# Performance work log

Hardware: AMD Instinct MI355X
Metric: run time of the kernel (lower is better)

## Reference

```python
import jax, jax.numpy as jnp
import numpy as np

T = 2048          # tokens (single causal prefill sequence)
H = 4096          # hidden_size
NH = 32           # num query heads
NKV = 8           # num kv heads (GQA)
HD = H // NH      # head_dim = 128
ROPE_THETA = 500000.0
Q_SIZE = NH * HD
KV_SIZE = NKV * HD


def setup_inputs() -> dict:
    key = jax.random.key(0)
    k1, k2, k3 = jax.random.split(key, 3)
    return {
        "positions": jnp.arange(T, dtype=jnp.int32),
        "hidden_states": jax.random.normal(k1, (T, H), dtype=jnp.float32) * 0.02,
        "w_qkv": jax.random.normal(k2, (H, Q_SIZE + 2 * KV_SIZE), dtype=jnp.float32) * (1.0 / np.sqrt(H)),
        "w_o": jax.random.normal(k3, (Q_SIZE, H), dtype=jnp.float32) * (1.0 / np.sqrt(Q_SIZE)),
    }


def _apply_rope(x, positions):
    # x: [T, heads, HD]; neox-style (non-interleaved) RoPE as in get_rope
    half = HD // 2
    inv_freq = 1.0 / (ROPE_THETA ** (jnp.arange(0, half, dtype=jnp.float32) / half * 1.0))
    # note: standard llama uses arange(0, HD, 2)/HD == arange(half)/half
    freqs = positions.astype(jnp.float32)[:, None] * inv_freq[None, :]   # [T, half]
    cos = jnp.cos(freqs)[:, None, :]  # [T, 1, half]
    sin = jnp.sin(freqs)[:, None, :]
    x1, x2 = x[..., :half], x[..., half:]
    return jnp.concatenate([x1 * cos - x2 * sin, x2 * cos + x1 * sin], axis=-1).astype(x.dtype)


def reference(positions, hidden_states, w_qkv, w_o):
    # qkv_proj (no bias)
    qkv = hidden_states @ w_qkv                               # [T, 6144]
    q, k, v = jnp.split(qkv, [Q_SIZE, Q_SIZE + KV_SIZE], axis=-1)
    q = q.reshape(T, NH, HD)
    k = k.reshape(T, NKV, HD)
    v = v.reshape(T, NKV, HD)

    # fused RoPE on q and k (k would be written rotated into the KV cache)
    q = _apply_rope(q, positions)
    k = _apply_rope(k, positions)

    # GQA: expand kv heads to query heads
    group = NH // NKV
    k_rep = jnp.repeat(k, group, axis=1)                      # [T, NH, HD]
    v_rep = jnp.repeat(v, group, axis=1)

    scale = HD ** -0.5
    scores = jnp.einsum('qhd,shd->hqs', q, k_rep) * scale     # [NH, T, T]
    causal = jnp.tril(jnp.ones((T, T), dtype=bool))
    scores = jnp.where(causal[None], scores, jnp.finfo(scores.dtype).min)
    probs = jax.nn.softmax(scores, axis=-1)
    attn = jnp.einsum('hqs,shd->qhd', probs, v_rep)           # [T, NH, HD]

    out = attn.reshape(T, Q_SIZE) @ w_o                       # o_proj
    return out
```

## Files before the change

kernel.cpp:

```cpp
#include <hip/hip_runtime.h>
#include <cstdint>
#include <cstddef>

#define T_SEQ 2048
#define H_DIM 4096
#define NH 32
#define NKV 8
#define HD 128
#define QKV_N 6144
#define Q_SIZE 4096
#define KV_SIZE 1024

typedef __attribute__((ext_vector_type(8))) short bf16x8;
typedef __attribute__((ext_vector_type(4))) short short4v;
typedef __attribute__((ext_vector_type(4))) float f32x4;

__device__ __forceinline__ short f2bf(float f) {
  union { float f; uint32_t u; } v; v.f = f;
  uint32_t r = v.u + 0x7fffu + ((v.u >> 16) & 1u);
  return (short)(r >> 16);
}

__device__ __forceinline__ void gload_lds16(const void* g, void* l) {
  __builtin_amdgcn_global_load_lds((const __attribute__((address_space(1))) void*)g,
                                   (__attribute__((address_space(3))) void*)l,
                                   16, 0, 0);
}

__global__ __launch_bounds__(256) void cvt_bf16_kernel(const float* __restrict__ in,
                                                       short* __restrict__ out, int n4) {
  int i = blockIdx.x * 256 + threadIdx.x;
  if (i < n4) {
    float4 v = ((const float4*)in)[i];
    short4v s;
    s.x = f2bf(v.x); s.y = f2bf(v.y); s.z = f2bf(v.z); s.w = f2bf(v.w);
    ((short4v*)out)[i] = s;
  }
}

__global__ __launch_bounds__(256) void transpose_cvt_kernel(const float* __restrict__ in,
                                                            short* __restrict__ out,
                                                            int rows, int cols) {
  __shared__ float tile[32][33];
  int bx = blockIdx.x * 32;
  int by = blockIdx.y * 32;
  int x = threadIdx.x, y = threadIdx.y;
#pragma unroll
  for (int i = 0; i < 32; i += 8)
    tile[y + i][x] = in[(size_t)(by + y + i) * cols + bx + x];
  __syncthreads();
#pragma unroll
  for (int i = 0; i < 32; i += 8)
    out[(size_t)(bx + y + i) * rows + by + x] = f2bf(tile[x][y + i]);
}

__global__ __launch_bounds__(256) void gemm_bt_kernel(const short* __restrict__ A,
                                                      const short* __restrict__ Bt,
                                                      float* __restrict__ C,
                                                      int M, int N, int K) {
  __shared__ short As[128 * 32];
  __shared__ short Bs[128 * 32];
  int tid = threadIdx.x;
  int w = tid >> 6, lane = tid & 63;
  int quad = lane >> 4, l16 = lane & 15;
  int wm = (w >> 1) * 64, wn = (w & 1) * 64;
  int bm = blockIdx.y * 128, bn = blockIdx.x * 128;
  f32x4 acc[4][4] = {};
  for (int kk = 0; kk < K; kk += 32) {
    __syncthreads();
#pragma unroll
    for (int p = 0; p < 2; ++p) {
      int e = (p * 256 + tid) * 8;
      int row = e >> 5, kc = e & 31;
      gload_lds16(A + (size_t)(bm + row) * K + kk + kc, As + e);
      gload_lds16(Bt + (size_t)(bn + row) * K + kk + kc, Bs + e);
    }
    __syncthreads();
    bf16x8 af[4], bfr[4];
#pragma unroll
    for (int mi = 0; mi < 4; ++mi)
      af[mi] = *(const bf16x8*)(As + (wm + mi * 16 + l16) * 32 + quad * 8);
#pragma unroll
    for (int ni = 0; ni < 4; ++ni)
      bfr[ni] = *(const bf16x8*)(Bs + (wn + ni * 16 + l16) * 32 + quad * 8);
#pragma unroll
    for (int mi = 0; mi < 4; ++mi)
#pragma unroll
      for (int ni = 0; ni < 4; ++ni)
        acc[mi][ni] = __builtin_amdgcn_mfma_f32_16x16x32_bf16(af[mi], bfr[ni], acc[mi][ni], 0, 0, 0);
  }
#pragma unroll
  for (int mi = 0; mi < 4; ++mi)
#pragma unroll
    for (int ni = 0; ni < 4; ++ni) {
      int r0 = bm + wm + mi * 16 + quad * 4;
      int c0 = bn + wn + ni * 16 + l16;
#pragma unroll
      for (int r = 0; r < 4; ++r)
        C[(size_t)(r0 + r) * N + c0] = acc[mi][ni][r];
    }
}

__global__ __launch_bounds__(256) void qkv_gemm_kernel(const short* __restrict__ A,
                                                       const short* __restrict__ Bt,
                                                       const int* __restrict__ positions,
                                                       short* __restrict__ qb,
                                                       short* __restrict__ kb,
                                                       short* __restrict__ vt) {
  __shared__ short As[128 * 32];
  __shared__ short Bs[128 * 32];
  const int K = H_DIM;
  int tid = threadIdx.x;
  int w = tid >> 6, lane = tid & 63;
  int quad = lane >> 4, l16 = lane & 15;
  int wm = (w >> 1) * 64;
  int cgb = (w & 1) * 32;
  int cb = blockIdx.x;
  int bm = blockIdx.y * 128, bn = cb * 128;
  f32x4 acc[4][4] = {};
  for (int kk = 0; kk < K; kk += 32) {
    __syncthreads();
#pragma unroll
    for (int p = 0; p < 2; ++p) {
      int e = (p * 256 + tid) * 8;
      int row = e >> 5, kc = e & 31;
      gload_lds16(A + (size_t)(bm + row) * K + kk + kc, As + e);
      gload_lds16(Bt + (size_t)(bn + row) * K + kk + kc, Bs + e);
    }
    __syncthreads();
    bf16x8 af[4], bfr[4];
#pragma unroll
    for (int mi = 0; mi < 4; ++mi)
      af[mi] = *(const bf16x8*)(As + (wm + mi * 16 + l16) * 32 + quad * 8);
#pragma unroll
    for (int nj = 0; nj < 4; ++nj) {
      int cg = cgb + (nj & 1) * 16 + (nj >> 1) * 64;
      bfr[nj] = *(const bf16x8*)(Bs + (cg + l16) * 32 + quad * 8);
    }
#pragma unroll
    for (int mi = 0; mi < 4; ++mi)
#pragma unroll
      for (int nj = 0; nj < 4; ++nj)
        acc[mi][nj] = __builtin_amdgcn_mfma_f32_16x16x32_bf16(af[mi], bfr[nj], acc[mi][nj], 0, 0, 0);
  }
  const float scale2 = 0.08838834764831845f * 1.4426950408889634f;
  if (cb < NH + NKV) {
    short* dstbase;
    float qs;
    if (cb < NH) { dstbase = qb + (size_t)cb * T_SEQ * HD; qs = scale2; }
    else         { dstbase = kb + (size_t)(cb - NH) * T_SEQ * HD; qs = 1.0f; }
    float invf[2];
#pragma unroll
    for (int nj = 0; nj < 2; ++nj)
      invf[nj] = exp2f(-(float)(cgb + nj * 16 + l16) * 0.29580575889569017f);
#pragma unroll
    for (int mi = 0; mi < 4; ++mi) {
#pragma unroll
      for (int r = 0; r < 4; ++r) {
        int t = bm + wm + mi * 16 + quad * 4 + r;
        float pos = (float)positions[t];
#pragma unroll
        for (int nj = 0; nj < 2; ++nj) {
          float f = pos * invf[nj];
          float sn, cs;
          __sincosf(f, &sn, &cs);
          float x1 = acc[mi][nj][r], x2 = acc[mi][nj + 2][r];
          float o1 = (x1 * cs - x2 * sn) * qs;
          float o2 = (x2 * cs + x1 * sn) * qs;
          int d = cgb + nj * 16 + l16;
          dstbase[(size_t)t * HD + d] = f2bf(o1);
          dstbase[(size_t)t * HD + d + 64] = f2bf(o2);
        }
      }
    }
  } else {
    short* vb = vt + (size_t)(cb - NH - NKV) * HD * T_SEQ;
#pragma unroll
    for (int mi = 0; mi < 4; ++mi)
#pragma unroll
      for (int nj = 0; nj < 4; ++nj) {
        int d = cgb + (nj & 1) * 16 + (nj >> 1) * 64 + l16;
        int t0 = bm + wm + mi * 16 + quad * 4;
        short4v pk;
        pk.x = f2bf(acc[mi][nj][0]); pk.y = f2bf(acc[mi][nj][1]);
        pk.z = f2bf(acc[mi][nj][2]); pk.w = f2bf(acc[mi][nj][3]);
        *(short4v*)(vb + (size_t)d * T_SEQ + t0) = pk;
      }
  }
}

#define PS_STR 72
__global__ __launch_bounds__(256, 2) void flash_kernel(const short* __restrict__ qb,
                                                       const short* __restrict__ kb,
                                                       const short* __restrict__ vt,
                                                       short* __restrict__ attn) {
  __shared__ short Ks[64 * 128];
  __shared__ short Vs[128 * 64];
  __shared__ short Ps[8][16 * PS_STR];
  int c = (int)gridDim.x - 1 - (int)blockIdx.x;
  int h = blockIdx.y;
  int kvh = h >> 2;
  int tid = threadIdx.x;
  int w = tid >> 6, lane = tid & 63;
  int quad = lane >> 4, l16 = lane & 15;
  int qrow0w = c * 128 + w * 32;

  const short* kbh = kb + (size_t)kvh * T_SEQ * HD;
  const short* vth = vt + (size_t)kvh * HD * T_SEQ;

  bf16x8 qf[2][4];
#pragma unroll
  for (int g = 0; g < 2; ++g) {
    const short* qbase = qb + ((size_t)h * T_SEQ + qrow0w + g * 16 + l16) * HD + quad * 8;
#pragma unroll
    for (int dk = 0; dk < 4; ++dk) qf[g][dk] = *(const bf16x8*)(qbase + dk * 32);
  }
  f32x4 o[2][8] = {};
  float lp[2] = {0.0f, 0.0f};

  int ktmax_blk = 2 * c + 2;
  int ktmax_w = 2 * c + 1 + (w >> 1);

  for (int kt = 0; kt < ktmax_blk; ++kt) {
    int kpos0 = kt * 64;
    __syncthreads();
#pragma unroll
    for (int p4 = 0; p4 < 4; ++p4) {
      int e = p4 * 256 + tid;
      int kr = e >> 4, kp = e & 15;
      gload_lds16(kbh + (size_t)(kpos0 + kr) * HD + ((kp ^ (kr & 7)) * 8), Ks + e * 8);
      int vd = e >> 3, vp = e & 7;
      gload_lds16(vth + (size_t)vd * T_SEQ + kpos0 + ((vp ^ (vd & 7)) * 8), Vs + e * 8);
    }
    __syncthreads();
    if (kt >= ktmax_w) continue;

    f32x4 s[2][4] = {};
#pragma unroll
    for (int mi = 0; mi < 4; ++mi) {
      int kr = mi * 16 + l16;
      const short* kfb = Ks + kr * 128;
      int sw = kr & 7;
#pragma unroll
      for (int dk = 0; dk < 4; ++dk) {
        bf16x8 kf = *(const bf16x8*)(kfb + (((dk * 4 + quad) ^ sw) * 8));
        s[0][mi] = __builtin_amdgcn_mfma_f32_16x16x32_bf16(kf, qf[0][dk], s[0][mi], 0, 0, 0);
        s[1][mi] = __builtin_amdgcn_mfma_f32_16x16x32_bf16(kf, qf[1][dk], s[1][mi], 0, 0, 0);
      }
    }
#pragma unroll
    for (int g = 0; g < 2; ++g) {
      int qr = qrow0w + g * 16 + l16;
      bool need_mask = (kpos0 + 63 > qrow0w + g * 16);
#pragma unroll
      for (int mi = 0; mi < 4; ++mi) {
        float p0, p1, p2, p3;
        if (need_mask) {
          int kp = kpos0 + mi * 16 + quad * 4;
          p0 = exp2f((kp + 0 > qr) ? -1e30f : s[g][mi][0]);
          p1 = exp2f((kp + 1 > qr) ? -1e30f : s[g][mi][1]);
          p2 = exp2f((kp + 2 > qr) ? -1e30f : s[g][mi][2]);
          p3 = exp2f((kp + 3 > qr) ? -1e30f : s[g][mi][3]);
        } else {
          p0 = exp2f(s[g][mi][0]); p1 = exp2f(s[g][mi][1]);
          p2 = exp2f(s[g][mi][2]); p3 = exp2f(s[g][mi][3]);
        }
        lp[g] += p0 + p1 + p2 + p3;
        short4v pk;
        pk.x = f2bf(p0); pk.y = f2bf(p1); pk.z = f2bf(p2); pk.w = f2bf(p3);
        *(short4v*)(&Ps[w * 2 + g][l16 * PS_STR + mi * 16 + quad * 4]) = pk;
      }
    }
#pragma unroll
    for (int kf2 = 0; kf2 < 2; ++kf2) {
      bf16x8 pf0 = *(const bf16x8*)(&Ps[w * 2 + 0][l16 * PS_STR + kf2 * 32 + quad * 8]);
      bf16x8 pf1 = *(const bf16x8*)(&Ps[w * 2 + 1][l16 * PS_STR + kf2 * 32 + quad * 8]);
#pragma unroll
      for (int ni = 0; ni < 8; ++ni) {
        int vd = ni * 16 + l16;
        bf16x8 vf = *(const bf16x8*)(Vs + vd * 64 + (((kf2 * 4 + quad) ^ (vd & 7)) * 8));
        o[0][ni] = __builtin_amdgcn_mfma_f32_16x16x32_bf16(vf, pf0, o[0][ni], 0, 0, 0);
        o[1][ni] = __builtin_amdgcn_mfma_f32_16x16x32_bf16(vf, pf1, o[1][ni], 0, 0, 0);
      }
    }
  }
#pragma unroll
  for (int g = 0; g < 2; ++g) {
    float lt = lp[g];
    lt += __shfl_xor(lt, 16, 64);
    lt += __shfl_xor(lt, 32, 64);
    float rl = 1.0f / lt;
    short* dst = attn + (size_t)(qrow0w + g * 16 + l16) * Q_SIZE + h * HD + quad * 4;
#pragma unroll
    for (int ni = 0; ni < 8; ++ni) {
      short4v ov;
      ov.x = f2bf(o[g][ni][0] * rl); ov.y = f2bf(o[g][ni][1] * rl);
      ov.z = f2bf(o[g][ni][2] * rl); ov.w = f2bf(o[g][ni][3] * rl);
      *(short4v*)(dst + ni * 16) = ov;
    }
  }
}

extern "C" void kernel_launch(void* const* d_in, const int* in_sizes, int n_in,
                              void* d_out, int out_size, void* d_ws, size_t ws_size,
                              hipStream_t stream) {
  const int* positions = (const int*)d_in[0];
  const float* hidden  = (const float*)d_in[1];
  const float* w_qkv   = (const float*)d_in[2];
  const float* w_o     = (const float*)d_in[3];
  float* out = (float*)d_out;

  char* p = (char*)d_ws;
  short* hA    = (short*)p;               short* attn = hA;
  p += (size_t)T_SEQ * H_DIM * 2;
  short* wqkvT = (short*)p;               short* woT = wqkvT;
  p += (size_t)QKV_N * H_DIM * 2;
  short* qb = (short*)p;
  short* kb = qb + (size_t)NH * T_SEQ * HD;
  short* vt = kb + (size_t)NKV * T_SEQ * HD;

  cvt_bf16_kernel<<<dim3(T_SEQ * H_DIM / 4 / 256), 256, 0, stream>>>(hidden, hA, T_SEQ * H_DIM / 4);
  transpose_cvt_kernel<<<dim3(QKV_N / 32, H_DIM / 32), dim3(32, 8), 0, stream>>>(w_qkv, wqkvT, H_DIM, QKV_N);
  qkv_gemm_kernel<<<dim3(QKV_N / 128, T_SEQ / 128), 256, 0, stream>>>(hA, wqkvT, positions, qb, kb, vt);
  transpose_cvt_kernel<<<dim3(H_DIM / 32, H_DIM / 32), dim3(32, 8), 0, stream>>>(w_o, woT, H_DIM, H_DIM);
  flash_kernel<<<dim3(T_SEQ / 128, NH), 256, 0, stream>>>(qb, kb, vt, attn);
  gemm_bt_kernel<<<dim3(H_DIM / 128, T_SEQ / 128), 256, 0, stream>>>(attn, woT, out, T_SEQ, H_DIM, H_DIM);
}
```

Measured before the change: 593.6 us.

## Split-K the output projection and stage Q/K RoPE stores through LDS

The o_proj GEMM now splits K in two across a third grid dimension, doubling block count from 512 to 1024 so the CUs are better filled. The second half writes to a workspace buffer, and a separate add kernel sums the two partials. The QKV GEMM epilogue also writes rotated Q/K values into padded shared memory and then stores 16-byte rows, instead of scattered 2-byte global writes. Costs are an extra 32 MB partial write and read plus one more launch, and extra barriers in the epilogue.

After: 592.5 us. No clear change (-0.2%).

```diff
diff --git a/kernel.cpp b/kernel.cpp
--- a/kernel.cpp
+++ b/kernel.cpp
@@ -54,10 +54,11 @@
     out[(size_t)(bx + y + i) * rows + by + x] = f2bf(tile[x][y + i]);
 }
 
-__global__ __launch_bounds__(256) void gemm_bt_kernel(const short* __restrict__ A,
+__global__ __launch_bounds__(256) void gemm_bt_splitk(const short* __restrict__ A,
                                                       const short* __restrict__ Bt,
-                                                      float* __restrict__ C,
-                                                      int M, int N, int K) {
+                                                      float* __restrict__ C0,
+                                                      float* __restrict__ C1,
+                                                      int M, int N, int Khalf) {
   __shared__ short As[128 * 32];
   __shared__ short Bs[128 * 32];
   int tid = threadIdx.x;
@@ -65,8 +66,12 @@
   int quad = lane >> 4, l16 = lane & 15;
   int wm = (w >> 1) * 64, wn = (w & 1) * 64;
   int bm = blockIdx.y * 128, bn = blockIdx.x * 128;
+  int z = blockIdx.z;
+  float* C = z ? C1 : C0;
+  int kbeg = z * Khalf, kend = kbeg + Khalf;
+  const int K = 2 * Khalf;
   f32x4 acc[4][4] = {};
-  for (int kk = 0; kk < K; kk += 32) {
+  for (int kk = kbeg; kk < kend; kk += 32) {
     __syncthreads();
 #pragma unroll
     for (int p = 0; p < 2; ++p) {
@@ -99,6 +104,17 @@
       for (int r = 0; r < 4; ++r)
         C[(size_t)(r0 + r) * N + c0] = acc[mi][ni][r];
     }
+}
+
+__global__ __launch_bounds__(256) void add_kernel(float* __restrict__ out,
+                                                  const float* __restrict__ p1, int n4) {
+  int i = blockIdx.x * 256 + threadIdx.x;
+  if (i < n4) {
+    float4 a = ((const float4*)out)[i];
+    float4 b = ((const float4*)p1)[i];
+    a.x += b.x; a.y += b.y; a.z += b.z; a.w += b.w;
+    ((float4*)out)[i] = a;
+  }
 }
 
 __global__ __launch_bounds__(256) void qkv_gemm_kernel(const short* __restrict__ A,
@@ -107,8 +123,9 @@
                                                        short* __restrict__ qb,
                                                        short* __restrict__ kb,
                                                        short* __restrict__ vt) {
-  __shared__ short As[128 * 32];
-  __shared__ short Bs[128 * 32];
+  __shared__ short Sh[8448];
+  short* As = Sh;
+  short* Bs = Sh + 4096;
   const int K = H_DIM;
   int tid = threadIdx.x;
   int w = tid >> 6, lane = tid & 63;
@@ -143,6 +160,7 @@
       for (int nj = 0; nj < 4; ++nj)
         acc[mi][nj] = __builtin_amdgcn_mfma_f32_16x16x32_bf16(af[mi], bfr[nj], acc[mi][nj], 0, 0, 0);
   }
+  __syncthreads();
   const float scale2 = 0.08838834764831845f * 1.4426950408889634f;
   if (cb < NH + NKV) {
     short* dstbase;
@@ -154,24 +172,37 @@
     for (int nj = 0; nj < 2; ++nj)
       invf[nj] = exp2f(-(float)(cgb + nj * 16 + l16) * 0.29580575889569017f);
 #pragma unroll
-    for (int mi = 0; mi < 4; ++mi) {
-#pragma unroll
-      for (int r = 0; r < 4; ++r) {
-        int t = bm + wm + mi * 16 + quad * 4 + r;
-        float pos = (float)positions[t];
-#pragma unroll
-        for (int nj = 0; nj < 2; ++nj) {
-          float f = pos * invf[nj];
-          float sn, cs;
-          __sincosf(f, &sn, &cs);
-          float x1 = acc[mi][nj][r], x2 = acc[mi][nj + 2][r];
-          float o1 = (x1 * cs - x2 * sn) * qs;
-          float o2 = (x2 * cs + x1 * sn) * qs;
-          int d = cgb + nj * 16 + l16;
-          dstbase[(size_t)t * HD + d] = f2bf(o1);
-          dstbase[(size_t)t * HD + d + 64] = f2bf(o2);
+    for (int half = 0; half < 2; ++half) {
+      if ((w >> 1) == half) {
+#pragma unroll
+        for (int mi = 0; mi < 4; ++mi) {
+#pragma unroll
+          for (int r = 0; r < 4; ++r) {
+            int lr = mi * 16 + quad * 4 + r;
+            int t = bm + half * 64 + lr;
+            float pos = (float)positions[t];
+#pragma unroll
+            for (int nj = 0; nj < 2; ++nj) {
+              float f = pos * invf[nj];
+              float sn, cs;
+              __sincosf(f, &sn, &cs);
+              float x1 = acc[mi][nj][r], x2 = acc[mi][nj + 2][r];
+              int d = cgb + nj * 16 + l16;
+              Sh[lr * 132 + d]      = f2bf((x1 * cs - x2 * sn) * qs);
+              Sh[lr * 132 + d + 64] = f2bf((x2 * cs + x1 * sn) * qs);
+            }
+          }
         }
       }
+      __syncthreads();
+#pragma unroll
+      for (int p = 0; p < 4; ++p) {
+        int e = p * 256 + tid;
+        int r2 = e >> 4, c8 = (e & 15) * 8;
+        bf16x8 val = *(const bf16x8*)(Sh + r2 * 132 + c8);
+        *(bf16x8*)(dstbase + (size_t)(bm + half * 64 + r2) * HD + c8) = val;
+      }
+      __syncthreads();
     }
   } else {
     short* vb = vt + (size_t)(cb - NH - NKV) * HD * T_SEQ;
@@ -312,10 +343,10 @@
 
   char* p = (char*)d_ws;
   short* hA    = (short*)p;               short* attn = hA;
-  p += (size_t)T_SEQ * H_DIM * 2;
-  short* wqkvT = (short*)p;               short* woT = wqkvT;
-  p += (size_t)QKV_N * H_DIM * 2;
-  short* qb = (short*)p;
+  short* wqkvT = (short*)(p + ((size_t)16 << 20));
+  short* woT   = wqkvT;
+  float* P1    = (float*)(p + ((size_t)48 << 20));
+  short* qb    = (short*)(p + ((size_t)64 << 20));
   short* kb = qb + (size_t)NH * T_SEQ * HD;
   short* vt = kb + (size_t)NKV * T_SEQ * HD;
 
@@ -324,5 +355,6 @@
   qkv_gemm_kernel<<<dim3(QKV_N / 128, T_SEQ / 128), 256, 0, stream>>>(hA, wqkvT, positions, qb, kb, vt);
   transpose_cvt_kernel<<<dim3(H_DIM / 32, H_DIM / 32), dim3(32, 8), 0, stream>>>(w_o, woT, H_DIM, H_DIM);
   flash_kernel<<<dim3(T_SEQ / 128, NH), 256, 0, stream>>>(qb, kb, vt, attn);
-  gemm_bt_kernel<<<dim3(H_DIM / 128, T_SEQ / 128), 256, 0, stream>>>(attn, woT, out, T_SEQ, H_DIM, H_DIM);
-}
+  gemm_bt_splitk<<<dim3(H_DIM / 128, T_SEQ / 128, 2), 256, 0, stream>>>(attn, woT, out, P1, T_SEQ, H_DIM, H_DIM / 2);
+  add_kernel<<<dim3(T_SEQ * H_DIM / 4 / 256), 256, 0, stream>>>(out, P1, T_SEQ * H_DIM / 4);
+}
```
